# Kernel optimization log

Hardware: AMD Instinct MI355X
Metric: run time of the kernel (lower is better)

Reference implementation:

```python
import jax, jax.numpy as jnp
import numpy as np

B, S, D, H = 4, 2048, 1024, 16
HD = D // H
EPS = 1e-7  # K.epsilon()


def setup_inputs() -> dict:
    key = jax.random.key(0)
    ks = jax.random.split(key, 5)
    scale = 1.0 / np.sqrt(D)  # keep projections numerically tame (glorot-ish)
    return {
        "x": jax.random.normal(ks[0], (B, S, D), dtype=jnp.float32),
        "Wq": jax.random.normal(ks[1], (D, D), dtype=jnp.float32) * scale,
        "bq": jnp.zeros((D,), dtype=jnp.float32),
        "Wk": jax.random.normal(ks[2], (D, D), dtype=jnp.float32) * scale,
        "bk": jnp.zeros((D,), dtype=jnp.float32),
        "Wv": jax.random.normal(ks[3], (D, D), dtype=jnp.float32) * scale,
        "bv": jnp.zeros((D,), dtype=jnp.float32),
        "Wo": jax.random.normal(ks[4], (D, D), dtype=jnp.float32) * scale,
        "bo": jnp.zeros((D,), dtype=jnp.float32),
    }


def _split_heads(t):
    # [B,S,D] -> [B,H,S,HD]
    return t.reshape(B, S, H, HD).transpose(0, 2, 1, 3)


def reference(x, Wq, bq, Wk, bk, Wv, bv, Wo, bo):
    relu = jax.nn.relu
    # projections with post-activation (keras layer applies activation to each mapping)
    q = _split_heads(relu(x @ Wq + bq))
    k = _split_heads(relu(x @ Wk + bk))
    v = _split_heads(relu(x @ Wv + bv))
    # scaled dot-product scores, scale = sqrt(head_dim)
    e = jnp.einsum("bhqd,bhkd->bhqk", q, k) / jnp.sqrt(jnp.asarray(HD, x.dtype))
    # exp with row max over ALL keys (before masking), as in the source
    e = jnp.exp(e - jnp.max(e, axis=-1, keepdims=True))
    # history_only: multiplicative causal mask applied AFTER exp
    causal = (jnp.arange(S)[None, :] <= jnp.arange(S)[:, None]).astype(x.dtype)
    e = e * causal  # broadcasts over [B,H,S,S]
    a = e / (jnp.sum(e, axis=-1, keepdims=True) + EPS)
    ctx = jnp.einsum("bhqk,bhkd->bhqd", a, v)
    y = ctx.transpose(0, 2, 1, 3).reshape(B, S, D)  # merge heads
    return relu(y @ Wo + bo)
```

## Files before the change

kernel.cpp:

```cpp
#include <hip/hip_runtime.h>
#include <hip/hip_bf16.h>
#include <cstdint>
#include <cstddef>

#define B_  4
#define S_  2048
#define D_  1024
#define H_  16
#define HD_ 64

typedef _Float16 half8  __attribute__((ext_vector_type(8)));
typedef _Float16 half4v __attribute__((ext_vector_type(4)));
typedef _Float16 half2v __attribute__((ext_vector_type(2)));
typedef float    f32x4  __attribute__((ext_vector_type(4)));
typedef unsigned int uint2v __attribute__((ext_vector_type(2)));
typedef unsigned int uint4v __attribute__((ext_vector_type(4)));

__device__ __forceinline__ void async_copy16(const void* g, void* l) {
    __builtin_amdgcn_global_load_lds(
        (const __attribute__((address_space(1))) unsigned int*)g,
        (__attribute__((address_space(3))) unsigned int*)l,
        16, 0, 0);
}

__device__ __forceinline__ half8 hscale8(half8 v, _Float16 s) {
    #pragma unroll
    for (int i = 0; i < 8; ++i) v[i] *= s;
    return v;
}

__device__ __forceinline__ unsigned int pack2(float a, float b) {
    half2v h = { (_Float16)a, (_Float16)b };
    return __builtin_bit_cast(unsigned int, h);
}


__global__ void cast_x_kernel(const float4* __restrict__ in, half4v* __restrict__ out, int n4) {
    int i = blockIdx.x * 256 + threadIdx.x;
    if (i < n4) {
        float4 v = in[i];
        half4v h = { (_Float16)v.x, (_Float16)v.y, (_Float16)v.z, (_Float16)v.w };
        out[i] = h;
    }
}

__global__ void transpose_cast4_kernel(
    const float* __restrict__ W0, const float* __restrict__ W1,
    const float* __restrict__ W2, const float* __restrict__ W3,
    _Float16* __restrict__ T0, _Float16* __restrict__ T1,
    _Float16* __restrict__ T2, _Float16* __restrict__ T3)
{
    __shared__ float tile[32][33];
    const float* Wsel[4] = { W0, W1, W2, W3 };
    _Float16*    Tsel[4] = { T0, T1, T2, T3 };
    const float* W  = Wsel[blockIdx.z];
    _Float16*    Wt = Tsel[blockIdx.z];
    const int bn = blockIdx.x * 32, bk = blockIdx.y * 32;
    const int tx = threadIdx.x, ty = threadIdx.y;
    #pragma unroll
    for (int i = 0; i < 32; i += 8)
        tile[ty + i][tx] = W[(size_t)(bk + ty + i) * D_ + bn + tx];
    __syncthreads();
    #pragma unroll
    for (int i = 0; i < 32; i += 8)
        Wt[(size_t)(bn + ty + i) * D_ + bk + tx] = (_Float16)tile[tx][ty + i];
}

template<int OUT_MODE>
__global__ __launch_bounds__(256, 2) void gemm_bt_kernel(
    const _Float16* __restrict__ A, const _Float16* __restrict__ Bt,
    const float* __restrict__ b0, const float* __restrict__ b1,
    const float* __restrict__ b2,
    void* __restrict__ C0, void* __restrict__ C1, void* __restrict__ C2,
    int M, int N, int K)
{
    __shared__ _Float16 As[128 * 64];
    __shared__ _Float16 Bs[128 * 64];
    const int tid  = threadIdx.x;
    const int wid  = tid >> 6, lane = tid & 63;
    const int lr   = lane & 15, lq = lane >> 4;
    const int m0   = blockIdx.x * 128, n0 = blockIdx.y * 128;
    const int wm   = (wid >> 1) * 64, wn = (wid & 1) * 64;
    const int srow = tid >> 3;
    const int csw  = ((tid & 7) ^ (srow & 7)) * 8;

    f32x4 acc[4][4] = {};

    for (int k0 = 0; k0 < K; k0 += 64) {
        __syncthreads();
        #pragma unroll
        for (int i = 0; i < 4; ++i) {
            async_copy16(A  + (size_t)(m0 + i * 32 + srow) * K + k0 + csw,
                         (char*)As + (i * 256 + wid * 64) * 16);
            async_copy16(Bt + (size_t)(n0 + i * 32 + srow) * K + k0 + csw,
                         (char*)Bs + (i * 256 + wid * 64) * 16);
        }
        __syncthreads();
        #pragma unroll
        for (int ks = 0; ks < 2; ++ks) {
            half8 af[4], bf[4];
            #pragma unroll
            for (int t = 0; t < 4; ++t) {
                af[t] = *(const half8*)(As + (wm + t * 16 + lr) * 64 + (((ks * 4 + lq) ^ (lr & 7)) * 8));
                bf[t] = *(const half8*)(Bs + (wn + t * 16 + lr) * 64 + (((ks * 4 + lq) ^ (lr & 7)) * 8));
            }
            #pragma unroll
            for (int mt = 0; mt < 4; ++mt)
                #pragma unroll
                for (int nt = 0; nt < 4; ++nt)
                    acc[mt][nt] = __builtin_amdgcn_mfma_f32_16x16x32_f16(
                        af[mt], bf[nt], acc[mt][nt], 0, 0, 0);
        }
    }

    const int seg = (OUT_MODE == 3) ? (n0 >> 10) : 0;
    const float* bp = (OUT_MODE == 3) ? (seg == 0 ? b0 : (seg == 1 ? b1 : b2)) : b0;

    #pragma unroll
    for (int mt = 0; mt < 4; ++mt) {
        const int row = m0 + wm + mt * 16 + lq * 4;
        #pragma unroll
        for (int nt = 0; nt < 4; ++nt) {
            const int col = n0 + wn + nt * 16 + lr;
            const int cl  = (OUT_MODE == 3) ? (col & 1023) : col;
            const float bb = bp[cl];
            if (OUT_MODE == 3 && seg == 2) {
                const int b = row >> 11, sq = row & 2047;
                const int h = cl >> 6, hd = cl & 63;
                half4v o;
                #pragma unroll
                for (int r = 0; r < 4; ++r) {
                    float v = acc[mt][nt][r] + bb;
                    o[r] = (_Float16)(v > 0.0f ? v : 0.0f);
                }
                *(half4v*)((_Float16*)C2 +
                           ((size_t)(b * 16 + h) * 64 + hd) * S_ + sq) = o;
            } else if (OUT_MODE == 3) {
                _Float16* dst = (_Float16*)(seg ? C1 : C0);
                #pragma unroll
                for (int r = 0; r < 4; ++r) {
                    float v = acc[mt][nt][r] + bb;
                    dst[(size_t)(row + r) * 1024 + cl] = (_Float16)(v > 0.0f ? v : 0.0f);
                }
            } else {
                #pragma unroll
                for (int r = 0; r < 4; ++r) {
                    float v = acc[mt][nt][r] + bb;
                    ((float*)C0)[(size_t)(row + r) * N + col] = v > 0.0f ? v : 0.0f;
                }
            }
        }
    }
}

__global__ __launch_bounds__(256, 2) void attn_kernel(
    const _Float16* __restrict__ Qg, const _Float16* __restrict__ Kg,
    const _Float16* __restrict__ Vtg, _Float16* __restrict__ Y)
{
    __shared__ _Float16 Ks[2][64 * 64];
    __shared__ _Float16 Vt[2][64 * 64];

    const int i  = blockIdx.x;
    const int bh = ((i & 7) << 3) | (i >> 6);
    const int p  = (i >> 3) & 7;
    const int b  = bh >> 4, h = bh & 15;
    const int tid = threadIdx.x, wid = tid >> 6, lane = tid & 63;
    const int lr = lane & 15, lq = lane >> 4;

    const size_t base  = ((size_t)b * S_) * D_ + (size_t)h * HD_;
    const _Float16* Vh = Vtg + (size_t)bh * 64 * S_;

    const int srow = tid >> 3;
    const int csw  = ((tid & 7) ^ (srow & 7)) * 8;

    const int L = 128 * p, Hh = 1920 - 128 * p;
    const int qb[4] = { L + 16 * wid, L + 64 + 16 * wid,
                        Hh + 16 * wid, Hh + 64 + 16 * wid };
    const int dk[4] = { 2 * p, 2 * p + 1, 30 - 2 * p, 31 - 2 * p };
    const int nIter = 32 - 2 * p;

    half8 aq[4][2];
    #pragma unroll
    for (int f = 0; f < 4; ++f) {
        const _Float16* qp = Qg + base + (size_t)(qb[f] + lr) * D_;
        aq[f][0] = hscale8(*(const half8*)(qp + lq * 8),      (_Float16)0.18033688f);
        aq[f][1] = hscale8(*(const half8*)(qp + 32 + lq * 8), (_Float16)0.18033688f);
    }

    float lsum[4] = {};
    f32x4 O[4][4] = {};

    auto issue_tile = [&](int kb) {
        const int bufi = kb & 1;
        #pragma unroll
        for (int ii = 0; ii < 2; ++ii) {
            async_copy16(Kg + base + (size_t)(kb * 64 + ii * 32 + srow) * D_ + csw,
                         (char*)Ks[bufi] + (ii * 256 + wid * 64) * 16);
            async_copy16(Vh + (size_t)(ii * 32 + srow) * S_ + kb * 64 + csw,
                         (char*)Vt[bufi] + (ii * 256 + wid * 64) * 16);
        }
    };

    issue_tile(0);

    for (int kb = 0; kb < nIter; ++kb) {
        const int cur = kb & 1;
        __syncthreads();
        if (kb + 1 < nIter) issue_tile(kb + 1);

        const _Float16* Kc = Ks[cur];
        const _Float16* Vc = Vt[cur];

        half8 kf[2][4], bv[2][4];
        #pragma unroll
        for (int ks = 0; ks < 2; ++ks)
            #pragma unroll
            for (int tt = 0; tt < 4; ++tt) {
                kf[ks][tt] = *(const half8*)(Kc + (tt * 16 + lr) * 64 + (((ks * 4 + lq) ^ (lr & 7)) * 8));
                bv[ks][tt] = *(const half8*)(Vc + (tt * 16 + lr) * 64 + (((ks * 4 + lq) ^ (lr & 7)) * 8));
            }

        #pragma unroll
        for (int f = 0; f < 4; ++f) {
            if (kb > dk[f]) continue;

            f32x4 sc[4] = {};
            __builtin_amdgcn_s_setprio(1);
            #pragma unroll
            for (int ks = 0; ks < 2; ++ks)
                #pragma unroll
                for (int tt = 0; tt < 4; ++tt)
                    sc[tt] = __builtin_amdgcn_mfma_f32_16x16x32_f16(kf[ks][tt], aq[f][ks], sc[tt], 0, 0, 0);
            __builtin_amdgcn_s_setprio(0);

            const bool diag = (kb == dk[f]);
            const int qg = qb[f] + lr;
            const int kbase = kb * 64 + lq * 4;
            float sum = 0.0f;
            unsigned int pk[4][2];
            #pragma unroll
            for (int tt = 0; tt < 4; ++tt) {
                float ev[4];
                #pragma unroll
                for (int r = 0; r < 4; ++r) {
                    float e = __builtin_amdgcn_exp2f(fminf(sc[tt][r] - 5.770780f, 15.8696f));
                    if (diag)
                        e = (kbase + tt * 16 + r <= qg) ? e : 0.0f;
                    ev[r] = e;
                    sum += e;
                }
                pk[tt][0] = pack2(ev[0], ev[1]);
                pk[tt][1] = pack2(ev[2], ev[3]);
            }
            lsum[f] += sum;

            half8 ap[2];
            #pragma unroll
            for (int ks = 0; ks < 2; ++ks) {
                uint2v s1 = __builtin_amdgcn_permlane32_swap(pk[2 * ks][0], pk[2 * ks + 1][0], false, false);
                uint2v s2 = __builtin_amdgcn_permlane16_swap(s1[0], s1[1], false, false);
                uint2v u1 = __builtin_amdgcn_permlane32_swap(pk[2 * ks][1], pk[2 * ks + 1][1], false, false);
                uint2v u2 = __builtin_amdgcn_permlane16_swap(u1[0], u1[1], false, false);
                uint4v d = { s2[0], u2[0], s2[1], u2[1] };
                ap[ks] = __builtin_bit_cast(half8, d);
            }

            __builtin_amdgcn_s_setprio(1);
            #pragma unroll
            for (int ks = 0; ks < 2; ++ks)
                #pragma unroll
                for (int tt = 0; tt < 4; ++tt)
                    O[f][tt] = __builtin_amdgcn_mfma_f32_16x16x32_f16(ap[ks], bv[ks][tt], O[f][tt], 0, 0, 0);
            __builtin_amdgcn_s_setprio(0);
        }
    }

    #pragma unroll
    for (int f = 0; f < 4; ++f) {
        float tot = lsum[f];
        tot += __shfl_xor(tot, 16);
        tot += __shfl_xor(tot, 32);
        const int q0 = qb[f] + lq * 4;
        #pragma unroll
        for (int r = 0; r < 4; ++r) {
            const float inv = 1.0f / (__shfl(tot, lq * 4 + r) + 1e-7f);
            #pragma unroll
            for (int nt = 0; nt < 4; ++nt)
                Y[base + (size_t)(q0 + r) * D_ + nt * 16 + lr] = (_Float16)(O[f][nt][r] * inv);
        }
    }
}


extern "C" void kernel_launch(void* const* d_in, const int* in_sizes, int n_in,
                              void* d_out, int out_size, void* d_ws, size_t ws_size,
                              hipStream_t stream) {
    const float* x  = (const float*)d_in[0];
    const float* Wq = (const float*)d_in[1];
    const float* bq = (const float*)d_in[2];
    const float* Wk = (const float*)d_in[3];
    const float* bk = (const float*)d_in[4];
    const float* Wv = (const float*)d_in[5];
    const float* bv = (const float*)d_in[6];
    const float* Wo = (const float*)d_in[7];
    const float* bo = (const float*)d_in[8];

    char* ws = (char*)d_ws;
    _Float16* xh  = (_Float16*)ws;
    _Float16* wtq = (_Float16*)(ws + (size_t)16777216);
    _Float16* wtk = wtq + 1048576;
    _Float16* wtv = wtk + 1048576;
    _Float16* wto = wtv + 1048576;
    _Float16* Qh  = (_Float16*)(ws + (size_t)16777216 + 4 * (size_t)2097152);
    _Float16* Kh  = Qh + 8388608;
    _Float16* Vth = Kh + 8388608;
    _Float16* Yh  = Vth + 8388608;
    float* out = (float*)d_out;

    cast_x_kernel<<<8192, 256, 0, stream>>>((const float4*)x, (half4v*)xh, 2097152);
    transpose_cast4_kernel<<<dim3(32, 32, 4), dim3(32, 8), 0, stream>>>(
        Wq, Wk, Wv, Wo, wtq, wtk, wtv, wto);

    gemm_bt_kernel<3><<<dim3(64, 24), 256, 0, stream>>>(
        xh, wtq, bq, bk, bv, Qh, Kh, Vth, 8192, 3072, 1024);

    attn_kernel<<<512, 256, 0, stream>>>(Qh, Kh, Vth, Yh);

    gemm_bt_kernel<0><<<dim3(64, 8), 256, 0, stream>>>(
        Yh, wto, bo, bo, bo, out, out, out, 8192, 1024, 1024);
}
```

Measured before the change: 246.2 us.

## Double-buffer GEMM shared-memory tiles and fold exp offset into score accumulator

The projection GEMM now keeps two LDS buffers for the A and B tiles. It issues the async global-to-LDS load for the next K tile before running the MFMAs on the current one, and raises wave priority around the MFMA block, so memory latency is meant to overlap with matrix math. In the attention kernel, the constant exp2 offset now seeds the score accumulators instead of being subtracted per element, which removes one VALU op per score. The trade-off is twice the LDS per GEMM block, which may limit occupancy, and reliance on the barrier to wait for the outstanding async copies.

Measured after the change: 261.2 us. 6.1% more time.

```diff
diff --git a/kernel.cpp b/kernel.cpp
--- a/kernel.cpp
+++ b/kernel.cpp
@@ -74,8 +74,8 @@
     void* __restrict__ C0, void* __restrict__ C1, void* __restrict__ C2,
     int M, int N, int K)
 {
-    __shared__ _Float16 As[128 * 64];
-    __shared__ _Float16 Bs[128 * 64];
+    __shared__ _Float16 As[2][128 * 64];
+    __shared__ _Float16 Bs[2][128 * 64];
     const int tid  = threadIdx.x;
     const int wid  = tid >> 6, lane = tid & 63;
     const int lr   = lane & 15, lq = lane >> 4;
@@ -86,31 +86,44 @@
 
     f32x4 acc[4][4] = {};
 
-    for (int k0 = 0; k0 < K; k0 += 64) {
-        __syncthreads();
+    auto stage = [&](int k0, int buf) {
         #pragma unroll
         for (int i = 0; i < 4; ++i) {
             async_copy16(A  + (size_t)(m0 + i * 32 + srow) * K + k0 + csw,
-                         (char*)As + (i * 256 + wid * 64) * 16);
+                         (char*)As[buf] + (i * 256 + wid * 64) * 16);
             async_copy16(Bt + (size_t)(n0 + i * 32 + srow) * K + k0 + csw,
-                         (char*)Bs + (i * 256 + wid * 64) * 16);
-        }
-        __syncthreads();
+                         (char*)Bs[buf] + (i * 256 + wid * 64) * 16);
+        }
+    };
+
+    const int nk = K >> 6;
+    stage(0, 0);
+    asm volatile("s_waitcnt vmcnt(0)" ::: "memory");
+    __syncthreads();
+
+    for (int t = 0; t < nk; ++t) {
+        const int cur = t & 1;
+        if (t + 1 < nk) stage((t + 1) << 6, cur ^ 1);
+        const _Float16* Ac = As[cur];
+        const _Float16* Bc = Bs[cur];
         #pragma unroll
         for (int ks = 0; ks < 2; ++ks) {
             half8 af[4], bf[4];
             #pragma unroll
-            for (int t = 0; t < 4; ++t) {
-                af[t] = *(const half8*)(As + (wm + t * 16 + lr) * 64 + (((ks * 4 + lq) ^ (lr & 7)) * 8));
-                bf[t] = *(const half8*)(Bs + (wn + t * 16 + lr) * 64 + (((ks * 4 + lq) ^ (lr & 7)) * 8));
-            }
+            for (int t2 = 0; t2 < 4; ++t2) {
+                af[t2] = *(const half8*)(Ac + (wm + t2 * 16 + lr) * 64 + (((ks * 4 + lq) ^ (lr & 7)) * 8));
+                bf[t2] = *(const half8*)(Bc + (wn + t2 * 16 + lr) * 64 + (((ks * 4 + lq) ^ (lr & 7)) * 8));
+            }
+            __builtin_amdgcn_s_setprio(1);
             #pragma unroll
             for (int mt = 0; mt < 4; ++mt)
                 #pragma unroll
                 for (int nt = 0; nt < 4; ++nt)
                     acc[mt][nt] = __builtin_amdgcn_mfma_f32_16x16x32_f16(
                         af[mt], bf[nt], acc[mt][nt], 0, 0, 0);
-        }
+            __builtin_amdgcn_s_setprio(0);
+        }
+        __syncthreads();
     }
 
     const int seg = (OUT_MODE == 3) ? (n0 >> 10) : 0;
@@ -224,7 +237,10 @@
         for (int f = 0; f < 4; ++f) {
             if (kb > dk[f]) continue;
 
-            f32x4 sc[4] = {};
+            f32x4 sc[4];
+            #pragma unroll
+            for (int tt = 0; tt < 4; ++tt)
+                sc[tt] = f32x4{ -5.770780f, -5.770780f, -5.770780f, -5.770780f };
             __builtin_amdgcn_s_setprio(1);
             #pragma unroll
             for (int ks = 0; ks < 2; ++ks)
@@ -243,7 +259,7 @@
                 float ev[4];
                 #pragma unroll
                 for (int r = 0; r < 4; ++r) {
-                    float e = __builtin_amdgcn_exp2f(fminf(sc[tt][r] - 5.770780f, 15.8696f));
+                    float e = __builtin_amdgcn_exp2f(fminf(sc[tt][r], 15.8696f));
                     if (diag)
                         e = (kbase + tt * 16 + r <= qg) ? e : 0.0f;
                     ev[r] = e;
```

## Process two 64-key tiles per barrier with 128-key double-buffered LDS super-tiles

Applied to the files above, without the earlier changes.

The attention loop now loads 128-key super-tiles of K and transposed V into doubled LDS buffers and processes two 64-key sub-tiles per barrier, halving the number of __syncthreads and async-copy issue points. The constant max-shift is folded into the MFMA accumulator initialization, removing one subtract per score element. Block-to-pair mapping is reversed for the upper half of the grid to rebalance causal work across waves of blocks. LDS use per block doubles (64KB), which may limit occupancy relative to the launch bound of 2 blocks per CU.

After: 256.0 us. +4.0%, slower.

```diff
diff --git a/kernel.cpp b/kernel.cpp
--- a/kernel.cpp
+++ b/kernel.cpp
@@ -157,12 +157,13 @@
     const _Float16* __restrict__ Qg, const _Float16* __restrict__ Kg,
     const _Float16* __restrict__ Vtg, _Float16* __restrict__ Y)
 {
-    __shared__ _Float16 Ks[2][64 * 64];
-    __shared__ _Float16 Vt[2][64 * 64];
+    __shared__ _Float16 Ks[2][128 * 64];
+    __shared__ _Float16 Vt[2][64 * 128];
 
     const int i  = blockIdx.x;
     const int bh = ((i & 7) << 3) | (i >> 6);
-    const int p  = (i >> 3) & 7;
+    const int praw = (i >> 3) & 7;
+    const int p  = ((i >> 8) & 1) ? 7 - praw : praw;
     const int b  = bh >> 4, h = bh & 15;
     const int tid = threadIdx.x, wid = tid >> 6, lane = tid & 63;
     const int lr = lane & 15, lq = lane >> 4;
@@ -170,14 +171,16 @@
     const size_t base  = ((size_t)b * S_) * D_ + (size_t)h * HD_;
     const _Float16* Vh = Vtg + (size_t)bh * 64 * S_;
 
-    const int srow = tid >> 3;
-    const int csw  = ((tid & 7) ^ (srow & 7)) * 8;
+    const int krow = tid >> 3;
+    const int kcsw = ((tid & 7) ^ (krow & 7)) * 8;
+    const int vrow = tid >> 4;
+    const int vcsw = ((tid & 8) | ((tid & 7) ^ (vrow & 7))) * 8;
 
     const int L = 128 * p, Hh = 1920 - 128 * p;
     const int qb[4] = { L + 16 * wid, L + 64 + 16 * wid,
                         Hh + 16 * wid, Hh + 64 + 16 * wid };
     const int dk[4] = { 2 * p, 2 * p + 1, 30 - 2 * p, 31 - 2 * p };
-    const int nIter = 32 - 2 * p;
+    const int nSuper = 16 - p;
 
     half8 aq[4][2];
     #pragma unroll
@@ -190,88 +193,98 @@
     float lsum[4] = {};
     f32x4 O[4][4] = {};
 
-    auto issue_tile = [&](int kb) {
-        const int bufi = kb & 1;
-        #pragma unroll
-        for (int ii = 0; ii < 2; ++ii) {
-            async_copy16(Kg + base + (size_t)(kb * 64 + ii * 32 + srow) * D_ + csw,
+    auto issue_super = [&](int sb) {
+        const int bufi = sb & 1;
+        #pragma unroll
+        for (int ii = 0; ii < 4; ++ii) {
+            async_copy16(Kg + base + (size_t)(sb * 128 + ii * 32 + krow) * D_ + kcsw,
                          (char*)Ks[bufi] + (ii * 256 + wid * 64) * 16);
-            async_copy16(Vh + (size_t)(ii * 32 + srow) * S_ + kb * 64 + csw,
+            async_copy16(Vh + (size_t)(ii * 16 + vrow) * S_ + sb * 128 + vcsw,
                          (char*)Vt[bufi] + (ii * 256 + wid * 64) * 16);
         }
     };
 
-    issue_tile(0);
-
-    for (int kb = 0; kb < nIter; ++kb) {
-        const int cur = kb & 1;
+    issue_super(0);
+
+    for (int sb = 0; sb < nSuper; ++sb) {
+        const int cur = sb & 1;
         __syncthreads();
-        if (kb + 1 < nIter) issue_tile(kb + 1);
+        if (sb + 1 < nSuper) issue_super(sb + 1);
 
         const _Float16* Kc = Ks[cur];
         const _Float16* Vc = Vt[cur];
 
-        half8 kf[2][4], bv[2][4];
-        #pragma unroll
-        for (int ks = 0; ks < 2; ++ks)
-            #pragma unroll
-            for (int tt = 0; tt < 4; ++tt) {
-                kf[ks][tt] = *(const half8*)(Kc + (tt * 16 + lr) * 64 + (((ks * 4 + lq) ^ (lr & 7)) * 8));
-                bv[ks][tt] = *(const half8*)(Vc + (tt * 16 + lr) * 64 + (((ks * 4 + lq) ^ (lr & 7)) * 8));
+        #pragma unroll
+        for (int hh = 0; hh < 2; ++hh) {
+            const int kb = sb * 2 + hh;
+
+            half8 kf[2][4], bv[2][4];
+            #pragma unroll
+            for (int ks = 0; ks < 2; ++ks)
+                #pragma unroll
+                for (int tt = 0; tt < 4; ++tt) {
+                    kf[ks][tt] = *(const half8*)(Kc + (hh * 64 + tt * 16 + lr) * 64
+                                                 + (((ks * 4 + lq) ^ (lr & 7)) * 8));
+                    bv[ks][tt] = *(const half8*)(Vc + (tt * 16 + lr) * 128 + hh * 64
+                                                 + (((ks * 4 + lq) ^ (lr & 7)) * 8));
+                }
+
+            #pragma unroll
+            for (int f = 0; f < 4; ++f) {
+                if (kb > dk[f]) continue;
+
+                f32x4 sc[4];
+                #pragma unroll
+                for (int tt = 0; tt < 4; ++tt)
+                    sc[tt] = f32x4{ -5.770780f, -5.770780f, -5.770780f, -5.770780f };
+                __builtin_amdgcn_s_setprio(1);
+                #pragma unroll
+                for (int ks = 0; ks < 2; ++ks)
+                    #pragma unroll
+                    for (int tt = 0; tt < 4; ++tt)
+                        sc[tt] = __builtin_amdgcn_mfma_f32_16x16x32_f16(kf[ks][tt], aq[f][ks], sc[tt], 0, 0, 0);
+                __builtin_amdgcn_s_setprio(0);
+
+                const bool diag = (kb == dk[f]);
+                const int qg = qb[f] + lr;
+                const int kbase = kb * 64 + lq * 4;
+                float sum = 0.0f;
+                unsigned int pk[4][2];
+                #pragma unroll
+                for (int tt = 0; tt < 4; ++tt) {
+                    float ev[4];
+                    #pragma unroll
+                    for (int r = 0; r < 4; ++r) {
+                        float e = __builtin_amdgcn_exp2f(fminf(sc[tt][r], 15.8696f));
+                        if (diag)
+                            e = (kbase + tt * 16 + r <= qg) ? e : 0.0f;
+                        ev[r] = e;
+                        sum += e;
+                    }
+                    pk[tt][0] = pack2(ev[0], ev[1]);
+                    pk[tt][1] = pack2(ev[2], ev[3]);
+                }
+                lsum[f] += sum;
+
+                half8 ap[2];
+                #pragma unroll
+                for (int ks = 0; ks < 2; ++ks) {
+                    uint2v s1 = __builtin_amdgcn_permlane32_swap(pk[2 * ks][0], pk[2 * ks + 1][0], false, false);
+                    uint2v s2 = __builtin_amdgcn_permlane16_swap(s1[0], s1[1], false, false);
+                    uint2v u1 = __builtin_amdgcn_permlane32_swap(pk[2 * ks][1], pk[2 * ks + 1][1], false, false);
+                    uint2v u2 = __builtin_amdgcn_permlane16_swap(u1[0], u1[1], false, false);
+                    uint4v d = { s2[0], u2[0], s2[1], u2[1] };
+                    ap[ks] = __builtin_bit_cast(half8, d);
+                }
+
+                __builtin_amdgcn_s_setprio(1);
+                #pragma unroll
+                for (int ks = 0; ks < 2; ++ks)
+                    #pragma unroll
+                    for (int tt = 0; tt < 4; ++tt)
+                        O[f][tt] = __builtin_amdgcn_mfma_f32_16x16x32_f16(ap[ks], bv[ks][tt], O[f][tt], 0, 0, 0);
+                __builtin_amdgcn_s_setprio(0);
             }
-
-        #pragma unroll
-        for (int f = 0; f < 4; ++f) {
-            if (kb > dk[f]) continue;
-
-            f32x4 sc[4] = {};
-            __builtin_amdgcn_s_setprio(1);
-            #pragma unroll
-            for (int ks = 0; ks < 2; ++ks)
-                #pragma unroll
-                for (int tt = 0; tt < 4; ++tt)
-                    sc[tt] = __builtin_amdgcn_mfma_f32_16x16x32_f16(kf[ks][tt], aq[f][ks], sc[tt], 0, 0, 0);
-            __builtin_amdgcn_s_setprio(0);
-
-            const bool diag = (kb == dk[f]);
-            const int qg = qb[f] + lr;
-            const int kbase = kb * 64 + lq * 4;
-            float sum = 0.0f;
-            unsigned int pk[4][2];
-            #pragma unroll
-            for (int tt = 0; tt < 4; ++tt) {
-                float ev[4];
-                #pragma unroll
-                for (int r = 0; r < 4; ++r) {
-                    float e = __builtin_amdgcn_exp2f(fminf(sc[tt][r] - 5.770780f, 15.8696f));
-                    if (diag)
-                        e = (kbase + tt * 16 + r <= qg) ? e : 0.0f;
-                    ev[r] = e;
-                    sum += e;
-                }
-                pk[tt][0] = pack2(ev[0], ev[1]);
-                pk[tt][1] = pack2(ev[2], ev[3]);
-            }
-            lsum[f] += sum;
-
-            half8 ap[2];
-            #pragma unroll
-            for (int ks = 0; ks < 2; ++ks) {
-                uint2v s1 = __builtin_amdgcn_permlane32_swap(pk[2 * ks][0], pk[2 * ks + 1][0], false, false);
-                uint2v s2 = __builtin_amdgcn_permlane16_swap(s1[0], s1[1], false, false);
-                uint2v u1 = __builtin_amdgcn_permlane32_swap(pk[2 * ks][1], pk[2 * ks + 1][1], false, false);
-                uint2v u2 = __builtin_amdgcn_permlane16_swap(u1[0], u1[1], false, false);
-                uint4v d = { s2[0], u2[0], s2[1], u2[1] };
-                ap[ks] = __builtin_bit_cast(half8, d);
-            }
-
-            __builtin_amdgcn_s_setprio(1);
-            #pragma unroll
-            for (int ks = 0; ks < 2; ++ks)
-                #pragma unroll
-                for (int tt = 0; tt < 4; ++tt)
-                    O[f][tt] = __builtin_amdgcn_mfma_f32_16x16x32_f16(ap[ks], bv[ks][tt], O[f][tt], 0, 0, 0);
-            __builtin_amdgcn_s_setprio(0);
         }
     }
 
```
